# Optimization experiments

Hardware: AMD Instinct MI355X
Metric: run time of the kernel (lower is better)

The kernel has to match this reference:

```python
import jax, jax.numpy as jnp
import numpy as np

N_SRC = 100000
N_DST = 100000
E = 1250000
IN_SRC = 64
IN_DST = 64
OUT = 64


def setup_inputs() -> dict:
    key = jax.random.key(0)
    k = jax.random.split(key, 7)
    x_src = jax.random.normal(k[0], (N_SRC, IN_SRC), dtype=jnp.float32)
    x_dst = jax.random.normal(k[1], (N_DST, IN_DST), dtype=jnp.float32)
    edge_index_sd = jax.random.randint(k[2], (2, E), 0, N_SRC, dtype=jnp.int64)
    edge_weight = jax.random.uniform(k[3], (E,), dtype=jnp.float32)
    # Linear params (torch: y = x @ W.T + b), kaiming-ish scale
    W_nei = jax.random.normal(k[4], (OUT, IN_SRC), dtype=jnp.float32) / np.sqrt(IN_SRC)
    W_self = jax.random.normal(k[5], (OUT, IN_DST), dtype=jnp.float32) / np.sqrt(IN_DST)
    b_self = jax.random.normal(k[6], (OUT,), dtype=jnp.float32) / np.sqrt(IN_DST)
    return {"x_src": x_src, "x_dst": x_dst, "edge_index_sd": edge_index_sd,
            "edge_weight": edge_weight, "W_nei": W_nei, "W_self": W_self,
            "b_self": b_self}


def reference(x_src, x_dst, edge_index_sd, edge_weight, W_nei, W_self, b_self):
    src_idx = edge_index_sd[0]
    dst_idx = edge_index_sd[1]
    # self term: [N_dst, out]
    out = x_dst @ W_self.T + b_self
    # neighbor transform then gather per edge: [E, out]
    h_src = x_src @ W_nei.T
    msg = h_src[src_idx] * edge_weight[:, None]
    # scatter-add into dst rows
    out = out.at[dst_idx].add(msg)
    return out
```

## Files before the change

### kernel.cpp

```cpp
#include <hip/hip_runtime.h>

#define NN 100000
#define FD 64
#define NE 1250000

#define RPB 128
#define NBK ((NN + RPB - 1) / RPB)
#define NBP 1024
#define CAP 2048
#define CH  8192
#define NCH ((NE + CH - 1) / CH)
#define NTILE (NN / 16)

#define TPW 2
#define NWM (NTILE / TPW)
#define LIN_GRID ((2 * NWM + 3) / 4)
#define NEI_GRID ((NWM + 3) / 4)

#define SLP 68

typedef __attribute__((ext_vector_type(8))) short bf16x8;
typedef __attribute__((ext_vector_type(4))) float f32x4;

__device__ __forceinline__ short cvt_bf16(float f) {
    unsigned u = __float_as_uint(f);
    return (short)((u + 0x7FFFu + ((u >> 16) & 1u)) >> 16);
}
__device__ __forceinline__ float bf2f(unsigned short u) {
    return __uint_as_float(((unsigned)u) << 16);
}
__device__ __forceinline__ bf16x8 cvt8(const float4& a, const float4& b) {
    bf16x8 f;
    f[0]=cvt_bf16(a.x); f[1]=cvt_bf16(a.y); f[2]=cvt_bf16(a.z); f[3]=cvt_bf16(a.w);
    f[4]=cvt_bf16(b.x); f[5]=cvt_bf16(b.y); f[6]=cvt_bf16(b.z); f[7]=cvt_bf16(b.w);
    return f;
}

__global__ __launch_bounds__(256) void lin_nei(
    const float* __restrict__ x_src, const float* __restrict__ W_nei,
    unsigned short* __restrict__ hbuf, int* __restrict__ gcur)
{
    if (blockIdx.x == 0) {
        #pragma unroll
        for (int i = 0; i < NBP / 256; i++) gcur[threadIdx.x + i * 256] = 0;
    }
    const int lane = threadIdx.x & 63;
    const int m    = lane & 15;
    const int quad = lane >> 4;
    const int gw   = blockIdx.x * 4 + (threadIdx.x >> 6);
    if (gw >= NWM) return;

    const float* xb = x_src + (size_t)(gw * (TPW * 16) + m) * FD;
    float4 xv[TPW][4];
    #pragma unroll
    for (int t = 0; t < TPW; t++) {
        const float* xr = xb + (size_t)t * 16 * FD;
        xv[t][0] = *(const float4*)(xr + quad * 8);
        xv[t][1] = *(const float4*)(xr + quad * 8 + 4);
        xv[t][2] = *(const float4*)(xr + 32 + quad * 8);
        xv[t][3] = *(const float4*)(xr + 32 + quad * 8 + 4);
    }
    bf16x8 wf[2][4];
    #pragma unroll
    for (int kc = 0; kc < 2; kc++) {
        #pragma unroll
        for (int ct = 0; ct < 4; ct++) {
            const float4 w0 = *(const float4*)(W_nei + (ct * 16 + m) * FD + kc * 32 + quad * 8);
            const float4 w1 = *(const float4*)(W_nei + (ct * 16 + m) * FD + kc * 32 + quad * 8 + 4);
            wf[kc][ct] = cvt8(w0, w1);
        }
    }
    #pragma unroll
    for (int t = 0; t < TPW; t++) {
        const bf16x8 a0 = cvt8(xv[t][0], xv[t][1]);
        const bf16x8 a1 = cvt8(xv[t][2], xv[t][3]);
        const size_t rowbase = (size_t)(gw * (TPW * 16) + t * 16 + m) * FD;
        #pragma unroll
        for (int ct = 0; ct < 4; ct++) {
            f32x4 z = (f32x4){0.f, 0.f, 0.f, 0.f};
            z = __builtin_amdgcn_mfma_f32_16x16x32_bf16(wf[0][ct], a0, z, 0, 0, 0);
            z = __builtin_amdgcn_mfma_f32_16x16x32_bf16(wf[1][ct], a1, z, 0, 0, 0);
            ushort4 sv;
            sv.x = (unsigned short)cvt_bf16(z[0]);
            sv.y = (unsigned short)cvt_bf16(z[1]);
            sv.z = (unsigned short)cvt_bf16(z[2]);
            sv.w = (unsigned short)cvt_bf16(z[3]);
            *(ushort4*)(hbuf + rowbase + ct * 16 + quad * 4) = sv;
        }
    }
}

__global__ __launch_bounds__(1024) void kplace(
    const int* __restrict__ src, const int* __restrict__ dst,
    const float* __restrict__ ew, int* __restrict__ gcursor,
    int2* __restrict__ sp)
{
    __shared__ int cnt[NBP];
    const int t = threadIdx.x;
    if (t < NBP) cnt[t] = 0;
    __syncthreads();
    const int e0 = blockIdx.x * CH;

    int d[8];
    #pragma unroll
    for (int k = 0; k < 8; k++) {
        const int e = e0 + t + k * 1024;
        d[k] = (e < NE) ? dst[e] : -1;
    }
    #pragma unroll
    for (int k = 0; k < 8; k++)
        if (d[k] >= 0) atomicAdd(&cnt[d[k] >> 7], 1);
    __syncthreads();

    if (t < NBP) {
        const int c = cnt[t];
        cnt[t] = c ? (t * CAP + atomicAdd(&gcursor[t], c)) : 0;
    }
    __syncthreads();

    int s[8]; float w[8];
    #pragma unroll
    for (int k = 0; k < 8; k++) {
        const int e = e0 + t + k * 1024;
        if (e < NE) { s[k] = src[e]; w[k] = ew[e]; }
    }
    #pragma unroll
    for (int k = 0; k < 8; k++) {
        if (d[k] >= 0) {
            const int p = atomicAdd(&cnt[d[k] >> 7], 1);
            sp[p] = make_int2(s[k] | ((d[k] & (RPB - 1)) << 17),
                              __float_as_int(w[k]));
        }
    }
}

__global__ __launch_bounds__(512) void sort_gather(
    const int2* __restrict__ sp, const int* __restrict__ gcursor,
    const unsigned short* __restrict__ h, const float* __restrict__ x_dst,
    const float* __restrict__ W_self, const float* __restrict__ b_self,
    float* __restrict__ out)
{
    __shared__ int2 ebuf[CAP + 16];
    __shared__ int hist[RPB];
    __shared__ int rs[RPB];
    __shared__ int cur[RPB];
    __shared__ float self_lds[RPB * SLP];
    const int t = threadIdx.x;
    const int b = blockIdx.x;
    const int cnt = gcursor[b];
    const int s0 = b * CAP;
    const int row0 = b * RPB;
    const int wv   = t >> 6;
    const int lane = t & 63;
    const int m    = lane & 15;
    const int quad = lane >> 4;

    int xrow = row0 + wv * 16 + m;
    if (xrow >= NN) xrow = NN - 1;
    const float* xr = x_dst + (size_t)xrow * FD;
    const float4 x0 = *(const float4*)(xr + quad * 8);
    const float4 x1 = *(const float4*)(xr + quad * 8 + 4);
    const float4 x2 = *(const float4*)(xr + 32 + quad * 8);
    const float4 x3 = *(const float4*)(xr + 32 + quad * 8 + 4);

    if (t < RPB) hist[t] = 0;

    int2 ev[4]; int er[4];
    #pragma unroll
    for (int k = 0; k < 4; k++) {
        const int j = t + k * 512;
        if (j < cnt) { ev[k] = sp[s0 + j]; er[k] = ev[k].x >> 17; }
        else er[k] = -1;
    }
    __syncthreads();
    #pragma unroll
    for (int k = 0; k < 4; k++)
        if (er[k] >= 0) atomicAdd(&hist[er[k]], 1);
    __syncthreads();
    if (t < 64) {
        const int v0 = hist[2*t], v1 = hist[2*t + 1];
        const int s = v0 + v1;
        int inc = s;
        #pragma unroll
        for (int off = 1; off < 64; off <<= 1) {
            int u = __shfl_up(inc, off, 64);
            if (t >= off) inc += u;
        }
        const int ex = inc - s;
        rs[2*t]      = ex;       cur[2*t]     = ex;
        rs[2*t + 1]  = ex + v0;  cur[2*t + 1] = ex + v0;
    }
    __syncthreads();
    #pragma unroll
    for (int k = 0; k < 4; k++) {
        if (er[k] >= 0) {
            const int p = atomicAdd(&cur[er[k]], 1);
            ebuf[p] = ev[k];
        }
    }
    if (t < 16) ebuf[cnt + t] = make_int2(0, 0);

    {
        const bf16x8 a0 = cvt8(x0, x1);
        const bf16x8 a1 = cvt8(x2, x3);
        #pragma unroll
        for (int ct = 0; ct < 4; ct++) {
            const float4 w0 = *(const float4*)(W_self + (ct * 16 + m) * FD + quad * 8);
            const float4 w1 = *(const float4*)(W_self + (ct * 16 + m) * FD + quad * 8 + 4);
            const float4 w2 = *(const float4*)(W_self + (ct * 16 + m) * FD + 32 + quad * 8);
            const float4 w3 = *(const float4*)(W_self + (ct * 16 + m) * FD + 32 + quad * 8 + 4);
            f32x4 z = (f32x4){0.f, 0.f, 0.f, 0.f};
            z = __builtin_amdgcn_mfma_f32_16x16x32_bf16(cvt8(w0, w1), a0, z, 0, 0, 0);
            z = __builtin_amdgcn_mfma_f32_16x16x32_bf16(cvt8(w2, w3), a1, z, 0, 0, 0);
            const float4 bb = *(const float4*)(b_self + ct * 16 + quad * 4);
            float4 v;
            v.x = z[0] + bb.x; v.y = z[1] + bb.y;
            v.z = z[2] + bb.z; v.w = z[3] + bb.w;
            *(float4*)&self_lds[(wv * 16 + m) * SLP + ct * 16 + quad * 4] = v;
        }
    }
    __syncthreads();

    const unsigned tb = (unsigned)m << 3;
    #pragma unroll
    for (int i = 0; i < 4; i++) {
        const int r   = i * 32 + wv * 4 + quad;
        const int row = row0 + r;
        if (row >= NN) continue;
        const int rsr = rs[r];
        const int n   = hist[r];
        float a0 = 0.f, a1 = 0.f, a2 = 0.f, a3 = 0.f;
        for (int k = 0; k < n; k += 4) {
            int2 ed[4];
            #pragma unroll
            for (int j = 0; j < 4; j++)
                ed[j] = ebuf[rsr + k + j];
            uint2 dv[4]; float wv4[4];
            #pragma unroll
            for (int j = 0; j < 4; j++) {
                const unsigned off = (((unsigned)(ed[j].x & 0x1FFFF)) << 7) | tb;
                dv[j] = *(const uint2*)((const char*)h + off);
                wv4[j] = (k + j < n) ? __int_as_float(ed[j].y) : 0.f;
            }
            #pragma unroll
            for (int j = 0; j < 4; j++) {
                const float w = wv4[j];
                a0 = fmaf(__uint_as_float(dv[j].x << 16),         w, a0);
                a1 = fmaf(__uint_as_float(dv[j].x & 0xFFFF0000u), w, a1);
                a2 = fmaf(__uint_as_float(dv[j].y << 16),         w, a2);
                a3 = fmaf(__uint_as_float(dv[j].y & 0xFFFF0000u), w, a3);
            }
        }
        const float4 sv = *(const float4*)&self_lds[r * SLP + (m << 2)];
        float4 v;
        v.x = sv.x + a0; v.y = sv.y + a1; v.z = sv.z + a2; v.w = sv.w + a3;
        *(float4*)(out + (size_t)row * FD + (m << 2)) = v;
    }
}

__global__ __launch_bounds__(256) void lin_both(
    const float* __restrict__ x_src, const float* __restrict__ x_dst,
    const float* __restrict__ W_nei, const float* __restrict__ W_self,
    const float* __restrict__ b_self, unsigned short* __restrict__ hbuf,
    float* __restrict__ out)
{
    const int lane = threadIdx.x & 63;
    const int m    = lane & 15;
    const int quad = lane >> 4;
    const int gw   = blockIdx.x * 4 + (threadIdx.x >> 6);
    if (gw >= 2 * NWM) return;
    const bool self = gw >= NWM;
    const int  wm   = self ? gw - NWM : gw;
    const float* __restrict__ x = self ? x_dst : x_src;
    const float* __restrict__ W = self ? W_self : W_nei;

    const float* xb = x + (size_t)(wm * (TPW * 16) + m) * FD;
    float4 xv[TPW][4];
    #pragma unroll
    for (int t = 0; t < TPW; t++) {
        const float* xr = xb + (size_t)t * 16 * FD;
        xv[t][0] = *(const float4*)(xr + quad * 8);
        xv[t][1] = *(const float4*)(xr + quad * 8 + 4);
        xv[t][2] = *(const float4*)(xr + 32 + quad * 8);
        xv[t][3] = *(const float4*)(xr + 32 + quad * 8 + 4);
    }
    bf16x8 wf[2][4];
    #pragma unroll
    for (int kc = 0; kc < 2; kc++) {
        #pragma unroll
        for (int ct = 0; ct < 4; ct++) {
            const float4 w0 = *(const float4*)(W + (ct * 16 + m) * FD + kc * 32 + quad * 8);
            const float4 w1 = *(const float4*)(W + (ct * 16 + m) * FD + kc * 32 + quad * 8 + 4);
            wf[kc][ct] = cvt8(w0, w1);
        }
    }
    float4 bv[4];
    if (self) {
        #pragma unroll
        for (int ct = 0; ct < 4; ct++)
            bv[ct] = *(const float4*)(b_self + ct * 16 + quad * 4);
    }
    #pragma unroll
    for (int t = 0; t < TPW; t++) {
        const bf16x8 a0 = cvt8(xv[t][0], xv[t][1]);
        const bf16x8 a1 = cvt8(xv[t][2], xv[t][3]);
        f32x4 acc[4];
        #pragma unroll
        for (int ct = 0; ct < 4; ct++) {
            f32x4 z = (f32x4){0.f, 0.f, 0.f, 0.f};
            z = __builtin_amdgcn_mfma_f32_16x16x32_bf16(wf[0][ct], a0, z, 0, 0, 0);
            z = __builtin_amdgcn_mfma_f32_16x16x32_bf16(wf[1][ct], a1, z, 0, 0, 0);
            acc[ct] = z;
        }
        const size_t rowbase = (size_t)(wm * (TPW * 16) + t * 16 + m) * FD;
        if (!self) {
            #pragma unroll
            for (int ct = 0; ct < 4; ct++) {
                ushort4 sv;
                sv.x = (unsigned short)cvt_bf16(acc[ct][0]);
                sv.y = (unsigned short)cvt_bf16(acc[ct][1]);
                sv.z = (unsigned short)cvt_bf16(acc[ct][2]);
                sv.w = (unsigned short)cvt_bf16(acc[ct][3]);
                *(ushort4*)(hbuf + rowbase + ct * 16 + quad * 4) = sv;
            }
        } else {
            #pragma unroll
            for (int ct = 0; ct < 4; ct++) {
                float4 v;
                v.x = acc[ct][0] + bv[ct].x;
                v.y = acc[ct][1] + bv[ct].y;
                v.z = acc[ct][2] + bv[ct].z;
                v.w = acc[ct][3] + bv[ct].w;
                *(float4*)(out + rowbase + ct * 16 + quad * 4) = v;
            }
        }
    }
}

__global__ __launch_bounds__(256) void scatter_edges(
    const unsigned short* __restrict__ h, const int* __restrict__ eidx,
    const float* __restrict__ ew, float* __restrict__ out)
{
    const int lane  = threadIdx.x & 63;
    const int gwave = (int)((blockIdx.x * blockDim.x + threadIdx.x) >> 6);
    const int nwave = (int)((gridDim.x * blockDim.x) >> 6);
    const int* __restrict__ src = eidx;
    const int* __restrict__ dst = eidx + NE;
    for (int e = gwave; e < NE; e += nwave) {
        const float v = bf2f(h[(size_t)src[e] * FD + lane]) * ew[e];
        atomicAdd(out + (size_t)dst[e] * FD + lane, v);
    }
}

extern "C" void kernel_launch(void* const* d_in, const int* in_sizes, int n_in,
                              void* d_out, int out_size, void* d_ws, size_t ws_size,
                              hipStream_t stream)
{
    const float* x_src  = (const float*)d_in[0];
    const float* x_dst  = (const float*)d_in[1];
    const int*   eidx   = (const int*)  d_in[2];
    const float* ew     = (const float*)d_in[3];
    const float* W_nei  = (const float*)d_in[4];
    const float* W_self = (const float*)d_in[5];
    const float* b_self = (const float*)d_in[6];
    float* out = (float*)d_out;

    const int* src = eidx;
    const int* dst = eidx + NE;

    char* ws = (char*)d_ws;
    size_t off = 0;
    auto alloc = [&](size_t bytes) { char* p = ws + off; off += (bytes + 15) & ~(size_t)15; return p; };
    unsigned short* h = (unsigned short*)alloc((size_t)NN * FD * sizeof(unsigned short));
    int*  gcursor  = (int*) alloc((size_t)NBP * sizeof(int));
    int2* sp       = (int2*)alloc((size_t)NBP * CAP * sizeof(int2));
    const size_t need_main = off;
    const size_t need_h    = (size_t)NN * FD * sizeof(unsigned short);

    if (ws_size >= need_main) {
        lin_nei<<<NEI_GRID, 256, 0, stream>>>(x_src, W_nei, h, gcursor);
        kplace<<<NCH, 1024, 0, stream>>>(src, dst, ew, gcursor, sp);
        sort_gather<<<NBK, 512, 0, stream>>>(sp, gcursor, h, x_dst,
                                             W_self, b_self, out);
    } else if (ws_size >= need_h) {
        lin_both<<<LIN_GRID, 256, 0, stream>>>(x_src, x_dst, W_nei, W_self,
                                               b_self, h, out);
        scatter_edges<<<2048, 256, 0, stream>>>(h, eidx, ew, out);
    }
}
```

Measured before the change: 172.1 us.

## Keep self-term in MFMA registers and remap gather lanes to match

The self-linear result now stays in the MFMA output registers instead of being staged through a padded LDS buffer. The gather phase is remapped so each lane owns the same row and column slots as its MFMA accumulator. Each lane handles one destination row with four 8-byte loads per edge, replacing a layout where 16 lanes shared a row. This removes LDS traffic and a large LDS allocation, which may raise occupancy. In exchange, the 16 lanes of a quad group now walk different rows with unequal edge counts, adding divergence and less coalesced gathers.

```diff
diff --git a/kernel.cpp b/kernel.cpp
--- a/kernel.cpp
+++ b/kernel.cpp
@@ -16,8 +16,6 @@
 #define NWM (NTILE / TPW)
 #define LIN_GRID ((2 * NWM + 3) / 4)
 #define NEI_GRID ((NWM + 3) / 4)
-
-#define SLP 68
 
 typedef __attribute__((ext_vector_type(8))) short bf16x8;
 typedef __attribute__((ext_vector_type(4))) float f32x4;
@@ -144,7 +142,6 @@
     __shared__ int hist[RPB];
     __shared__ int rs[RPB];
     __shared__ int cur[RPB];
-    __shared__ float self_lds[RPB * SLP];
     const int t = threadIdx.x;
     const int b = blockIdx.x;
     const int cnt = gcursor[b];
@@ -200,61 +197,69 @@
     }
     if (t < 16) ebuf[cnt + t] = make_int2(0, 0);
 
+    f32x4 z[4];
     {
         const bf16x8 a0 = cvt8(x0, x1);
         const bf16x8 a1 = cvt8(x2, x3);
         #pragma unroll
         for (int ct = 0; ct < 4; ct++) {
-            const float4 w0 = *(const float4*)(W_self + (ct * 16 + m) * FD + quad * 8);
-            const float4 w1 = *(const float4*)(W_self + (ct * 16 + m) * FD + quad * 8 + 4);
-            const float4 w2 = *(const float4*)(W_self + (ct * 16 + m) * FD + 32 + quad * 8);
-            const float4 w3 = *(const float4*)(W_self + (ct * 16 + m) * FD + 32 + quad * 8 + 4);
-            f32x4 z = (f32x4){0.f, 0.f, 0.f, 0.f};
-            z = __builtin_amdgcn_mfma_f32_16x16x32_bf16(cvt8(w0, w1), a0, z, 0, 0, 0);
-            z = __builtin_amdgcn_mfma_f32_16x16x32_bf16(cvt8(w2, w3), a1, z, 0, 0, 0);
+            const float* wr = W_self + (ct * 16 + m) * FD;
+            const float4 w0 = *(const float4*)(wr + quad * 8);
+            const float4 w1 = *(const float4*)(wr + quad * 8 + 4);
+            const float4 w2 = *(const float4*)(wr + 32 + quad * 8);
+            const float4 w3 = *(const float4*)(wr + 32 + quad * 8 + 4);
+            f32x4 zz = (f32x4){0.f, 0.f, 0.f, 0.f};
+            zz = __builtin_amdgcn_mfma_f32_16x16x32_bf16(cvt8(w0, w1), a0, zz, 0, 0, 0);
+            zz = __builtin_amdgcn_mfma_f32_16x16x32_bf16(cvt8(w2, w3), a1, zz, 0, 0, 0);
             const float4 bb = *(const float4*)(b_self + ct * 16 + quad * 4);
+            z[ct][0] = zz[0] + bb.x;
+            z[ct][1] = zz[1] + bb.y;
+            z[ct][2] = zz[2] + bb.z;
+            z[ct][3] = zz[3] + bb.w;
+        }
+    }
+    __syncthreads();
+
+    const int r   = wv * 16 + m;
+    const int row = row0 + r;
+    const int n   = hist[r];
+    const int rsr = rs[r];
+    const unsigned cb = (unsigned)(quad << 3);
+    for (int k = 0; k < n; k += 4) {
+        int2 ed[4];
+        #pragma unroll
+        for (int j = 0; j < 4; j++)
+            ed[j] = ebuf[rsr + k + j];
+        uint2 dv[4][4]; float w4[4];
+        #pragma unroll
+        for (int j = 0; j < 4; j++) {
+            const char* hp = (const char*)h +
+                ((((unsigned)(ed[j].x & 0x1FFFF)) << 7) | cb);
+            dv[j][0] = *(const uint2*)(hp);
+            dv[j][1] = *(const uint2*)(hp + 32);
+            dv[j][2] = *(const uint2*)(hp + 64);
+            dv[j][3] = *(const uint2*)(hp + 96);
+            w4[j] = (k + j < n) ? __int_as_float(ed[j].y) : 0.f;
+        }
+        #pragma unroll
+        for (int j = 0; j < 4; j++) {
+            const float w = w4[j];
+            #pragma unroll
+            for (int ct = 0; ct < 4; ct++) {
+                z[ct][0] = fmaf(__uint_as_float(dv[j][ct].x << 16),         w, z[ct][0]);
+                z[ct][1] = fmaf(__uint_as_float(dv[j][ct].x & 0xFFFF0000u), w, z[ct][1]);
+                z[ct][2] = fmaf(__uint_as_float(dv[j][ct].y << 16),         w, z[ct][2]);
+                z[ct][3] = fmaf(__uint_as_float(dv[j][ct].y & 0xFFFF0000u), w, z[ct][3]);
+            }
+        }
+    }
+    if (row < NN) {
+        #pragma unroll
+        for (int ct = 0; ct < 4; ct++) {
             float4 v;
-            v.x = z[0] + bb.x; v.y = z[1] + bb.y;
-            v.z = z[2] + bb.z; v.w = z[3] + bb.w;
-            *(float4*)&self_lds[(wv * 16 + m) * SLP + ct * 16 + quad * 4] = v;
-        }
-    }
-    __syncthreads();
-
-    const unsigned tb = (unsigned)m << 3;
-    #pragma unroll
-    for (int i = 0; i < 4; i++) {
-        const int r   = i * 32 + wv * 4 + quad;
-        const int row = row0 + r;
-        if (row >= NN) continue;
-        const int rsr = rs[r];
-        const int n   = hist[r];
-        float a0 = 0.f, a1 = 0.f, a2 = 0.f, a3 = 0.f;
-        for (int k = 0; k < n; k += 4) {
-            int2 ed[4];
-            #pragma unroll
-            for (int j = 0; j < 4; j++)
-                ed[j] = ebuf[rsr + k + j];
-            uint2 dv[4]; float wv4[4];
-            #pragma unroll
-            for (int j = 0; j < 4; j++) {
-                const unsigned off = (((unsigned)(ed[j].x & 0x1FFFF)) << 7) | tb;
-                dv[j] = *(const uint2*)((const char*)h + off);
-                wv4[j] = (k + j < n) ? __int_as_float(ed[j].y) : 0.f;
-            }
-            #pragma unroll
-            for (int j = 0; j < 4; j++) {
-                const float w = wv4[j];
-                a0 = fmaf(__uint_as_float(dv[j].x << 16),         w, a0);
-                a1 = fmaf(__uint_as_float(dv[j].x & 0xFFFF0000u), w, a1);
-                a2 = fmaf(__uint_as_float(dv[j].y << 16),         w, a2);
-                a3 = fmaf(__uint_as_float(dv[j].y & 0xFFFF0000u), w, a3);
-            }
-        }
-        const float4 sv = *(const float4*)&self_lds[r * SLP + (m << 2)];
-        float4 v;
-        v.x = sv.x + a0; v.y = sv.y + a1; v.z = sv.z + a2; v.w = sv.w + a3;
-        *(float4*)(out + (size_t)row * FD + (m << 2)) = v;
+            v.x = z[ct][0]; v.y = z[ct][1]; v.z = z[ct][2]; v.w = z[ct][3];
+            *(float4*)(out + (size_t)row * FD + ct * 16 + (quad << 2)) = v;
+        }
     }
 }
 
@@ -307,10 +312,10 @@
         f32x4 acc[4];
         #pragma unroll
         for (int ct = 0; ct < 4; ct++) {
-            f32x4 z = (f32x4){0.f, 0.f, 0.f, 0.f};
-            z = __builtin_amdgcn_mfma_f32_16x16x32_bf16(wf[0][ct], a0, z, 0, 0, 0);
-            z = __builtin_amdgcn_mfma_f32_16x16x32_bf16(wf[1][ct], a1, z, 0, 0, 0);
-            acc[ct] = z;
+            f32x4 zz = (f32x4){0.f, 0.f, 0.f, 0.f};
+            zz = __builtin_amdgcn_mfma_f32_16x16x32_bf16(wf[0][ct], a0, zz, 0, 0, 0);
+            zz = __builtin_amdgcn_mfma_f32_16x16x32_bf16(wf[1][ct], a1, zz, 0, 0, 0);
+            acc[ct] = zz;
         }
         const size_t rowbase = (size_t)(wm * (TPW * 16) + t * 16 + m) * FD;
         if (!self) {
```

Measured after the change: 203.5 us. +18.2%, slower.
